# Performance work log

Measured on AMD Instinct MI355X. Metric: run time of the kernel, lower is better.

## Reference

```python
import jax, jax.numpy as jnp
import numpy as np
from jax import lax

B, C, H, W = 4, 3, 512, 512
PATCH = 64
STRIDE = 32
CHANS = [(3, 32), (32, 32), (32, 64), (64, 64), (64, 64), (64, 32), (32, 32), (32, 2)]


def _conv(x, w, b):
    y = lax.conv_general_dilated(x, w, (1, 1), [(1, 1), (1, 1)],
                                 dimension_numbers=('NCHW', 'OIHW', 'NCHW'))
    return y + b[None, :, None, None]


def _pool(x):  # MaxPool2d(2)
    return lax.reduce_window(x, -jnp.inf, lax.max, (1, 1, 2, 2), (1, 1, 2, 2), 'VALID')


def _up(x):  # Upsample(scale=2, bilinear, align_corners=False) == half-pixel resize
    b, c, h, w = x.shape
    return jax.image.resize(x, (b, c, 2 * h, 2 * w), 'bilinear')


def _flow_net(x, ws, bs):
    r = jax.nn.relu
    h = r(_conv(x, ws[0], bs[0]))
    h = r(_conv(h, ws[1], bs[1]))
    h = _pool(h)
    h = r(_conv(h, ws[2], bs[2]))
    h = r(_conv(h, ws[3], bs[3]))
    h = _pool(h)
    h = _up(h)
    h = r(_conv(h, ws[4], bs[4]))
    h = r(_conv(h, ws[5], bs[5]))
    h = _up(h)
    h = r(_conv(h, ws[6], bs[6]))
    return jnp.tanh(_conv(h, ws[7], bs[7]))  # [B,2,H,W]


def _bilinear_zeros(img, gx, gy):
    # img [C,H,W], gx/gy [N,P,P] in [-1,1]; grid_sample bilinear, zeros padding, align_corners=False
    Hh, Ww = img.shape[1], img.shape[2]
    ix = ((gx + 1.0) * Ww - 1.0) * 0.5
    iy = ((gy + 1.0) * Hh - 1.0) * 0.5
    x0 = jnp.floor(ix)
    y0 = jnp.floor(iy)
    wx1 = ix - x0
    wy1 = iy - y0

    def corner(xi, yi, wgt):
        valid = (xi >= 0) & (xi <= Ww - 1) & (yi >= 0) & (yi <= Hh - 1)
        xc = jnp.clip(xi, 0, Ww - 1).astype(jnp.int32)
        yc = jnp.clip(yi, 0, Hh - 1).astype(jnp.int32)
        return img[:, yc, xc] * (wgt * valid)[None]  # [C,N,P,P]

    return (corner(x0, y0, (1 - wx1) * (1 - wy1))
            + corner(x0 + 1, y0, wx1 * (1 - wy1))
            + corner(x0, y0 + 1, (1 - wx1) * wy1)
            + corner(x0 + 1, y0 + 1, wx1 * wy1))


def _forward(x, ws, bs, temp):
    b, c, h, w = x.shape
    flow = _flow_net(x, ws, bs)  # [B,2,H,W]
    gy, gx = jnp.meshgrid(jnp.linspace(-1.0, 1.0, h), jnp.linspace(-1.0, 1.0, w), indexing='ij')
    base = jnp.stack([gx, gy], axis=-1)  # [H,W,2] (x,y)
    deformed = base[None] + flow.transpose(0, 2, 3, 1) * temp  # [B,H,W,2]
    centers = deformed[:, ::STRIDE, ::STRIDE, :].reshape(b, -1, 2)  # [B,N,2]
    py, px = jnp.meshgrid(jnp.linspace(-1.0, 1.0, PATCH), jnp.linspace(-1.0, 1.0, PATCH), indexing='ij')
    pgx = centers[:, :, None, None, 0] + px[None, None] * (PATCH / w)  # [B,N,P,P]
    pgy = centers[:, :, None, None, 1] + py[None, None] * (PATCH / h)
    patches = jax.vmap(_bilinear_zeros)(x, pgx, pgy)  # [B,C,N,P,P]
    patches = patches.transpose(0, 2, 1, 3, 4)  # [B,N,C,P,P]
    return patches, flow, deformed


def setup_inputs() -> dict:
    key = jax.random.key(0)
    ks = jax.random.split(key, len(CHANS) + 1)
    d = {"x": jax.random.normal(ks[0], (B, C, H, W), jnp.float32)}
    for i, (ci, co) in enumerate(CHANS):
        d[f"w{i}"] = jax.random.normal(ks[i + 1], (co, ci, 3, 3), jnp.float32) * 0.01
        d[f"b{i}"] = jnp.zeros((co,), jnp.float32)
    d["temp"] = jnp.full((1,), 0.1, jnp.float32)
    return d


def reference(x, w0, b0, w1, b1, w2, b2, w3, b3, w4, b4, w5, b5, w6, b6, w7, b7, temp):
    ws = [w0, w1, w2, w3, w4, w5, w6, w7]
    bs = [b0, b1, b2, b3, b4, b5, b6, b7]
    return _forward(x, ws, bs, temp)
```

## Files before the change

### kernel.cpp

```cpp
#include <hip/hip_runtime.h>
#include <hip/hip_bf16.h>

typedef __hip_bfloat16 bf16;
typedef unsigned short ushort_t;
typedef __attribute__((ext_vector_type(8))) short short8;
typedef __attribute__((ext_vector_type(4))) float float4v;

#define BATCH 4
#define HH 512
#define WW 512

#define WO_L0 0
#define WO_L1 3072
#define WO_L2 12288
#define WO_L3 30720
#define WO_L4P 67584
#define WO_L5 215040
#define WO_L6P 233472
#define WO_L7 270336
#define WO_L4U 274944
#define WO_L6U 311808

__device__ __forceinline__ ushort_t f2bfu(float f) {
  __hip_bfloat16 h = __float2bfloat16(f);
  union { __hip_bfloat16 h; ushort_t u; } c;
  c.h = h;
  return c.u;
}
__device__ __forceinline__ float bfu2f(ushort_t u) {
  return __uint_as_float(((unsigned)u) << 16);
}

__device__ __forceinline__ void dma16(void* lds, const void* g) {
  __builtin_amdgcn_global_load_lds(
      (const __attribute__((address_space(1))) unsigned int*)g,
      (__attribute__((address_space(3))) unsigned int*)lds, 16, 0, 0);
}

__device__ __forceinline__ float upw(int k, int u) {
  int lo = k >> 1;
  float a = (k & 1) ? 0.25f : 0.75f;
  float b = (k & 1) ? 0.75f : 0.25f;
  return (u == lo) ? a : (u == lo + 1) ? b : 0.0f;
}

struct WP { const float* w[8]; };

__global__ __launch_bounds__(256) void prep_w(WP wp, bf16* __restrict__ dst) {
  const int job = blockIdx.y;
  const int e = blockIdx.x * 256 + threadIdx.x;
  if (job == 0) {
    if (e >= 3072) return;
    int c = e & 7;
    int o = (e >> 3) & 31;
    int g = (e >> 8) % 3;
    int tl = (e >> 8) / 3;
    int tap = g * 4 + tl;
    float v = 0.0f;
    if (tap < 9 && c < 3) v = wp.w[0][(o * 3 + c) * 9 + tap];
    dst[WO_L0 + e] = __float2bfloat16(v);
    return;
  }
  if (job == 4 || job == 6) {
    const int O = (job == 4) ? 64 : 32;
    const int I = O;
    const int NCH = I >> 5;
    const int n = 4 * NCH * 9 * O * 32;
    if (e >= n) return;
    int ic = e & 31;
    int o = (e >> 5) % O;
    int tap = (e / (32 * O)) % 9;
    int ch = (e / (9 * 32 * O)) % NCH;
    int ph = e / (NCH * 9 * 32 * O);
    int i = ch * 32 + ic;
    int u = tap / 3, v2 = tap - u * 3;
    int dy = ph >> 1, dx = ph & 1;
    const float* w = wp.w[job];
    float acc = 0.0f;
#pragma unroll
    for (int r = 0; r < 3; ++r) {
      float ry = upw(r + dy, u);
#pragma unroll
      for (int s = 0; s < 3; ++s)
        acc += w[(o * I + i) * 9 + r * 3 + s] * ry * upw(s + dx, v2);
    }
    dst[((job == 4) ? WO_L4P : WO_L6P) + e] = __float2bfloat16(acc);
    return;
  }
  int O, I, OP, off;
  const float* w;
  if (job == 1)      { O = 32; I = 32; OP = 32; off = WO_L1; w = wp.w[1]; }
  else if (job == 2) { O = 64; I = 32; OP = 64; off = WO_L2; w = wp.w[2]; }
  else if (job == 3) { O = 64; I = 64; OP = 64; off = WO_L3; w = wp.w[3]; }
  else if (job == 5) { O = 32; I = 64; OP = 32; off = WO_L5; w = wp.w[5]; }
  else if (job == 7) { O = 2;  I = 32; OP = 16; off = WO_L7; w = wp.w[7]; }
  else if (job == 8) { O = 64; I = 64; OP = 64; off = WO_L4U; w = wp.w[4]; }
  else               { O = 32; I = 32; OP = 32; off = WO_L6U; w = wp.w[6]; }
  const int NCH = I >> 5;
  const int n = NCH * 9 * OP * 32;
  if (e >= n) return;
  int ic = e & 31;
  int o = (e >> 5) % OP;
  int tap = (e / (32 * OP)) % 9;
  int ch = e / (9 * 32 * OP);
  int i = ch * 32 + ic;
  float v = 0.0f;
  if (o < O) v = w[(o * I + i) * 9 + tap];
  dst[off + e] = __float2bfloat16(v);
}

__global__ __launch_bounds__(256) void pack_x(const float* __restrict__ x,
                                              bf16* __restrict__ xp) {
  int i = blockIdx.x * 256 + threadIdx.x;
  if (i >= BATCH * HH * WW) return;
  int b = i / (HH * WW);
  int px = i - b * (HH * WW);
  union { uint4 v; ushort_t s[8]; } o;
  o.v = make_uint4(0, 0, 0, 0);
  const float* p = x + (long)b * 3 * HH * WW + px;
  o.s[0] = f2bfu(p[0]);
  o.s[1] = f2bfu(p[HH * WW]);
  o.s[2] = f2bfu(p[2 * HH * WW]);
  *(uint4*)&xp[(long)i * 8] = o.v;
}

__global__ __launch_bounds__(512) void conv01_k(
    const bf16* __restrict__ xp, const bf16* __restrict__ w0,
    const bf16* __restrict__ w1, const float* __restrict__ b0,
    const float* __restrict__ b1, bf16* __restrict__ out) {
  __shared__ alignas(16) bf16 xp_lds[720 * 8];
  __shared__ alignas(16) bf16 mid_lds[612 * 32];
  __shared__ alignas(16) bf16 w0_lds[3072];
  __shared__ alignas(16) bf16 w1_lds[9 * 32 * 32];
  const int tid = threadIdx.x;
  const int lane = tid & 63;
  const int wid = tid >> 6;
  const int lm = lane & 15;
  const int quad = lane >> 4;
  const int x0 = blockIdx.x * 16, y0 = blockIdx.y * 32;
  const int b = blockIdx.z;

  for (int u = tid; u < 720; u += 512) {
    int hy = u / 20, hx = u - hy * 20;
    int gy = y0 - 2 + hy, gx = x0 - 2 + hx;
    uint4 v = make_uint4(0, 0, 0, 0);
    if (gy >= 0 && gy < HH && gx >= 0 && gx < WW)
      v = *(const uint4*)(xp + (((long)b * HH + gy) * WW + gx) * 8);
    *(uint4*)&xp_lds[u * 8] = v;
  }
  if (tid < 384) *(uint4*)&w0_lds[tid * 8] = *(const uint4*)(w0 + tid * 8);
  for (int j = wid; j < 18; j += 8)
    dma16((char*)w1_lds + j * 1024, (const char*)w1 + j * 1024 + lane * 16);
  __syncthreads();

  for (int t = wid; t < 39; t += 8) {
    int px = t * 16 + lm;
    int pxc = min(px, 611);
    int hy = pxc / 18, hx = pxc - hy * 18;
    float4v acc0[2];
#pragma unroll
    for (int mt = 0; mt < 2; ++mt)
      acc0[mt] = *(const float4v*)(b0 + mt * 16 + quad * 4);
#pragma unroll
    for (int g = 0; g < 3; ++g) {
      int tap = g * 4 + quad;
      if (tap > 8) tap = 8;
      int r = (tap * 11) >> 5;
      int s = tap - r * 3;
      short8 bfr = *(const short8*)&xp_lds[((hy + r) * 20 + hx + s) * 8];
      short8 a0 = *(const short8*)&w0_lds[quad * 768 + (g * 32 + lm) * 8];
      short8 a1 = *(const short8*)&w0_lds[quad * 768 + (g * 32 + 16 + lm) * 8];
      acc0[0] = __builtin_amdgcn_mfma_f32_16x16x32_bf16(a0, bfr, acc0[0], 0, 0, 0);
      acc0[1] = __builtin_amdgcn_mfma_f32_16x16x32_bf16(a1, bfr, acc0[1], 0, 0, 0);
    }
    int gy = y0 - 1 + hy, gx = x0 - 1 + hx;
    bool inimg = (gy >= 0) && (gy < HH) && (gx >= 0) && (gx < WW);
    if (px < 612) {
#pragma unroll
      for (int mt = 0; mt < 2; ++mt) {
        union { uint2 v; ushort_t s2[4]; } pk;
#pragma unroll
        for (int r2 = 0; r2 < 4; ++r2)
          pk.s2[r2] = inimg ? f2bfu(fmaxf(acc0[mt][r2], 0.0f)) : (ushort_t)0;
        *(uint2*)&mid_lds[px * 32 + mt * 16 + quad * 4] = pk.v;
      }
    }
  }
  __syncthreads();

  float4v acc[2][4];
#pragma unroll
  for (int mt = 0; mt < 2; ++mt) {
    float4v bv = *(const float4v*)(b1 + mt * 16 + quad * 4);
#pragma unroll
    for (int nt = 0; nt < 4; ++nt) acc[mt][nt] = bv;
  }
#pragma unroll
  for (int tap = 0; tap < 9; ++tap) {
    const int r = tap / 3, s = tap - r * 3;
    short8 afrag[2], bfrag[4];
#pragma unroll
    for (int mt = 0; mt < 2; ++mt)
      afrag[mt] = *(const short8*)&w1_lds[(tap * 32 + mt * 16 + lm) * 32 + quad * 8];
#pragma unroll
    for (int nt = 0; nt < 4; ++nt) {
      int py = 4 * wid + nt;
      bfrag[nt] = *(const short8*)&mid_lds[((py + r) * 18 + lm + s) * 32 + quad * 8];
    }
#pragma unroll
    for (int mt = 0; mt < 2; ++mt)
#pragma unroll
      for (int nt = 0; nt < 4; ++nt)
        acc[mt][nt] = __builtin_amdgcn_mfma_f32_16x16x32_bf16(
            afrag[mt], bfrag[nt], acc[mt][nt], 0, 0, 0);
  }
  const int Ho = HH >> 1, Wo = WW >> 1;
#pragma unroll
  for (int mt = 0; mt < 2; ++mt) {
#pragma unroll
    for (int g = 0; g < 2; ++g) {
      float4v m;
#pragma unroll
      for (int r = 0; r < 4; ++r)
        m[r] = fmaxf(fmaxf(acc[mt][2 * g][r], acc[mt][2 * g + 1][r]), 0.0f);
#pragma unroll
      for (int r = 0; r < 4; ++r) m[r] = fmaxf(m[r], __shfl_xor(m[r], 1, 64));
      if ((lm & 1) == 0) {
        int pyo = (y0 >> 1) + 2 * wid + g;
        int pxo = (x0 >> 1) + (lm >> 1);
        union { uint2 v; ushort_t s[4]; } pk;
#pragma unroll
        for (int r = 0; r < 4; ++r) pk.s[r] = f2bfu(m[r]);
        *(uint2*)&out[(((long)b * Ho + pyo) * Wo + pxo) * 32 + mt * 16 +
                      quad * 4] = pk.v;
      }
    }
  }
}

template <int CIN, int COUT, int COUTR, int OUT_MODE>
__global__ __launch_bounds__(512) void conv_mfma(
    const bf16* __restrict__ in, const bf16* __restrict__ wt,
    const float* __restrict__ bias, void* __restrict__ out_, int H, int W,
    const float* __restrict__ temp, float* __restrict__ def) {
  constexpr int MT = COUT / 16;
  constexpr int CK = 32;
  __shared__ alignas(16) bf16 in_lds[612 * CK];
  __shared__ alignas(16) bf16 w_lds[9 * COUT * CK];
  const int tid = threadIdx.x;
  const int lane = tid & 63;
  const int wid = tid >> 6;
  const int lm = lane & 15;
  const int quad = lane >> 4;
  const int x0 = blockIdx.x * 16;
  const int y0 = blockIdx.y * 32;
  const int b = blockIdx.z;

  float4v acc[MT][4];
#pragma unroll
  for (int mt = 0; mt < MT; ++mt) {
    float4v bv;
    if constexpr (COUTR == COUT) {
      bv = *(const float4v*)(bias + mt * 16 + quad * 4);
    } else {
#pragma unroll
      for (int r = 0; r < 4; ++r) {
        int co = mt * 16 + quad * 4 + r;
        bv[r] = (co < COUTR) ? bias[co] : 0.0f;
      }
    }
#pragma unroll
    for (int nt = 0; nt < 4; ++nt) acc[mt][nt] = bv;
  }

  const bool interior =
      (x0 >= 1) && (x0 + 16 <= W - 1) && (y0 >= 1) && (y0 + 32 <= H - 1);
  for (int c0 = 0; c0 < CIN; c0 += CK) {
    if (interior) {
      for (int r = wid; r < 34; r += 8) {
        int gy = y0 - 1 + r;
        const bf16* gsrc = in + (((long)b * H + gy) * W + x0) * CIN + c0 +
                           (lane >> 2) * CIN + (lane & 3) * 8;
        dma16(&in_lds[(r * 18 + 1) * CK], gsrc);
      }
      if (tid < 272) {
        int r = tid >> 3;
        int side = (tid >> 2) & 1;
        int seg = tid & 3;
        int gx = side ? (x0 + 16) : (x0 - 1);
        int gy = y0 - 1 + r;
        uint4 v = *(const uint4*)(in + (((long)b * H + gy) * W + gx) * CIN +
                                  c0 + seg * 8);
        *(uint4*)&in_lds[(r * 18 + (side ? 17 : 0)) * CK + seg * 8] = v;
      }
    } else {
      for (int u = tid; u < 612 * 4; u += 512) {
        int px = u >> 2;
        int seg = u & 3;
        int hy = px / 18, hx = px - hy * 18;
        int gy = y0 - 1 + hy, gx = x0 - 1 + hx;
        uint4 v = make_uint4(0, 0, 0, 0);
        if (gy >= 0 && gy < H && gx >= 0 && gx < W)
          v = *(const uint4*)(in + (((long)b * H + gy) * W + gx) * CIN + c0 +
                              seg * 8);
        *(uint4*)&in_lds[px * CK + seg * 8] = v;
      }
    }
    {
      const char* wsrc = (const char*)(wt + (size_t)(c0 >> 5) * 9 * COUT * CK);
      constexpr int WCH = 9 * COUT * CK * 2 / 1024;
      for (int j = wid; j < WCH; j += 8)
        dma16((char*)w_lds + j * 1024, wsrc + j * 1024 + lane * 16);
    }
    __syncthreads();

#pragma unroll
    for (int tap = 0; tap < 9; ++tap) {
      const int r = tap / 3, s = tap - r * 3;
      short8 afrag[MT], bfrag[4];
#pragma unroll
      for (int mt = 0; mt < MT; ++mt)
        afrag[mt] =
            *(const short8*)&w_lds[(tap * COUT + mt * 16 + lm) * CK + quad * 8];
#pragma unroll
      for (int nt = 0; nt < 4; ++nt) {
        int py = 4 * wid + nt;
        bfrag[nt] =
            *(const short8*)&in_lds[((py + r) * 18 + lm + s) * CK + quad * 8];
      }
#pragma unroll
      for (int mt = 0; mt < MT; ++mt)
#pragma unroll
        for (int nt = 0; nt < 4; ++nt)
          acc[mt][nt] = __builtin_amdgcn_mfma_f32_16x16x32_bf16(
              afrag[mt], bfrag[nt], acc[mt][nt], 0, 0, 0);
    }
    __syncthreads();
  }

  if constexpr (OUT_MODE == 3) {
    bf16* out = (bf16*)out_;
    const int Ho = H >> 1, Wo = W >> 1;
#pragma unroll
    for (int mt = 0; mt < MT; ++mt) {
#pragma unroll
      for (int g = 0; g < 2; ++g) {
        float4v m;
#pragma unroll
        for (int r = 0; r < 4; ++r)
          m[r] = fmaxf(fmaxf(acc[mt][2 * g][r], acc[mt][2 * g + 1][r]), 0.0f);
#pragma unroll
        for (int r = 0; r < 4; ++r) m[r] = fmaxf(m[r], __shfl_xor(m[r], 1, 64));
        if ((lm & 1) == 0) {
          int pyo = (y0 >> 1) + 2 * wid + g;
          int pxo = (x0 >> 1) + (lm >> 1);
          union { uint2 v; ushort_t s[4]; } pk;
#pragma unroll
          for (int r = 0; r < 4; ++r) pk.s[r] = f2bfu(m[r]);
          *(uint2*)&out[(((long)b * Ho + pyo) * Wo + pxo) * COUT + mt * 16 +
                        quad * 4] = pk.v;
        }
      }
    }
  } else {
#pragma unroll
    for (int mt = 0; mt < MT; ++mt) {
#pragma unroll
      for (int nt = 0; nt < 4; ++nt) {
        int gy = y0 + 4 * wid + nt;
        int gx = x0 + lm;
        float4v v = acc[mt][nt];
        if constexpr (OUT_MODE == 0) {
          bf16* out = (bf16*)out_;
          union { uint2 v; ushort_t s[4]; } pk;
#pragma unroll
          for (int r = 0; r < 4; ++r) pk.s[r] = f2bfu(fmaxf(v[r], 0.0f));
          *(uint2*)&out[(((long)b * H + gy) * W + gx) * COUT + mt * 16 +
                        quad * 4] = pk.v;
        } else {
          float* out = (float*)out_;
          if (quad == 0) {
            float fx = tanhf(v[0]);
            float fy = tanhf(v[1]);
            out[(((long)b * 2 + 0) * H + gy) * (long)W + gx] = fx;
            out[(((long)b * 2 + 1) * H + gy) * (long)W + gx] = fy;
            float T = temp[0];
            float2 d;
            d.x = -1.0f + gx * (2.0f / 511.0f) + fx * T;
            d.y = -1.0f + gy * (2.0f / 511.0f) + fy * T;
            *(float2*)&def[(((long)b * HH + gy) * WW + gx) * 2] = d;
          }
        }
      }
    }
  }
}

template <int CIN, int COUT, bool PSPLIT>
__global__ __launch_bounds__(512) void conv_up(
    const bf16* __restrict__ in, const bf16* __restrict__ wtP,
    const bf16* __restrict__ wtU, const float* __restrict__ bias,
    bf16* __restrict__ out, int Ho, int Wo) {
  constexpr int MT = COUT / 16;
  constexpr int CK = 32;
  constexpr int WSZ = 9 * COUT * CK;
  constexpr int NWB = PSPLIT ? 1 : 2;
  __shared__ alignas(16) bf16 in_lds[612 * CK];
  __shared__ alignas(16) bf16 w_lds[NWB * WSZ];
  const int tid = threadIdx.x;
  const int lane = tid & 63;
  const int wid = tid >> 6;
  const int lm = lane & 15;
  const int quad = lane >> 4;
  const int Hs = Ho >> 1, Ws = Wo >> 1;
  const int nx = Ws >> 4, ny = Hs >> 5;
  const int bulkN = nx * ny;
  const int b = PSPLIT ? (blockIdx.z >> 2) : blockIdx.z;
  const int ph0 = PSPLIT ? (blockIdx.z & 3) : 0;
  const int t = blockIdx.x;

  if (t >= bulkN) {
    if (PSPLIT && ph0 != 0) return;
    const int G = Wo >> 4;
    int e = t - bulkN;
    int tx, ty;
    if (e < G) { ty = 0; tx = e; }
    else if (e < 2 * G) { ty = G - 1; tx = e - G; }
    else { int u = e - 2 * G; ty = 1 + (u >> 1); tx = (u & 1) ? (G - 1) : 0; }
    const int x0 = tx * 16, y0 = ty * 16;

    float4v acc[MT][4];
#pragma unroll
    for (int mt = 0; mt < MT; ++mt) {
      float4v bv = *(const float4v*)(bias + mt * 16 + quad * 4);
#pragma unroll
      for (int nt = 0; nt < 4; ++nt) acc[mt][nt] = bv;
    }

    for (int c0 = 0; c0 < CIN; c0 += CK) {
      for (int u = tid; u < 324 * 4; u += 512) {
        int px = u >> 2;
        int seg = u & 3;
        int hy = px / 18, hx = px - hy * 18;
        int gy = y0 - 1 + hy, gx = x0 - 1 + hx;
        uint4 o = make_uint4(0, 0, 0, 0);
        if (gy >= 0 && gy < Ho && gx >= 0 && gx < Wo) {
          int ys = (gy >> 1) - ((gy & 1) ? 0 : 1);
          int xs = (gx >> 1) - ((gx & 1) ? 0 : 1);
          float wy = (gy & 1) ? 0.25f : 0.75f;
          float wx = (gx & 1) ? 0.25f : 0.75f;
          int y0c = max(ys, 0), y1c = min(ys + 1, Hs - 1);
          int x0c = max(xs, 0), x1c = min(xs + 1, Ws - 1);
          const bf16* p = in + ((long)b * Hs * Ws) * CIN + c0 + seg * 8;
          union { uint4 v; ushort_t s[8]; } a00, a01, a10, a11, r;
          a00.v = *(const uint4*)(p + ((long)y0c * Ws + x0c) * CIN);
          a01.v = *(const uint4*)(p + ((long)y0c * Ws + x1c) * CIN);
          a10.v = *(const uint4*)(p + ((long)y1c * Ws + x0c) * CIN);
          a11.v = *(const uint4*)(p + ((long)y1c * Ws + x1c) * CIN);
#pragma unroll
          for (int j = 0; j < 8; ++j) {
            float f = (1.0f - wy) * ((1.0f - wx) * bfu2f(a00.s[j]) +
                                     wx * bfu2f(a01.s[j])) +
                      wy * ((1.0f - wx) * bfu2f(a10.s[j]) +
                            wx * bfu2f(a11.s[j]));
            r.s[j] = f2bfu(f);
          }
          o = r.v;
        }
        *(uint4*)&in_lds[px * CK + seg * 8] = o;
      }
      {
        const char* wsrc = (const char*)(wtU + (size_t)(c0 >> 5) * WSZ);
        constexpr int WCH = WSZ * 2 / 1024;
        for (int j = wid; j < WCH; j += 8)
          dma16((char*)w_lds + j * 1024, wsrc + j * 1024 + lane * 16);
      }
      __syncthreads();
      if (wid < 4) {
#pragma unroll
        for (int tap = 0; tap < 9; ++tap) {
          const int r = tap / 3, s = tap - r * 3;
          short8 afrag[MT], bfrag[4];
#pragma unroll
          for (int mt = 0; mt < MT; ++mt)
            afrag[mt] =
                *(const short8*)&w_lds[(tap * COUT + mt * 16 + lm) * CK + quad * 8];
#pragma unroll
          for (int nt = 0; nt < 4; ++nt) {
            int py = 4 * wid + nt;
            bfrag[nt] =
                *(const short8*)&in_lds[((py + r) * 18 + lm + s) * CK + quad * 8];
          }
#pragma unroll
          for (int mt = 0; mt < MT; ++mt)
#pragma unroll
            for (int nt = 0; nt < 4; ++nt)
              acc[mt][nt] = __builtin_amdgcn_mfma_f32_16x16x32_bf16(
                  afrag[mt], bfrag[nt], acc[mt][nt], 0, 0, 0);
        }
      }
      __syncthreads();
    }
    if (wid < 4) {
#pragma unroll
      for (int mt = 0; mt < MT; ++mt)
#pragma unroll
        for (int nt = 0; nt < 4; ++nt) {
          int gy = y0 + 4 * wid + nt;
          int gx = x0 + lm;
          union { uint2 v; ushort_t s[4]; } pk;
#pragma unroll
          for (int r = 0; r < 4; ++r)
            pk.s[r] = f2bfu(fmaxf(acc[mt][nt][r], 0.0f));
          *(uint2*)&out[(((long)b * Ho + gy) * Wo + gx) * COUT + mt * 16 +
                        quad * 4] = pk.v;
        }
    }
    return;
  }

  const int bx = t % nx, by = t / nx;
  const int xs0 = bx * 16, ys0 = by * 32;
  const bool interior = (bx >= 1) && (bx < nx - 1) && (by >= 1) && (by < ny - 1);

  if constexpr (!PSPLIT) {
    static_assert(CIN == CK, "non-split bulk path assumes single K chunk");
    if (interior) {
      for (int r = wid; r < 34; r += 8) {
        int gy = ys0 - 1 + r;
        const bf16* gsrc = in + (((long)b * Hs + gy) * Ws + xs0) * CIN +
                           (lane >> 2) * CIN + (lane & 3) * 8;
        dma16(&in_lds[(r * 18 + 1) * CK], gsrc);
      }
      if (tid < 272) {
        int r = tid >> 3;
        int side = (tid >> 2) & 1;
        int seg = tid & 3;
        int gx = side ? (xs0 + 16) : (xs0 - 1);
        int gy = ys0 - 1 + r;
        uint4 v = *(const uint4*)(in + (((long)b * Hs + gy) * Ws + gx) * CIN +
                                  seg * 8);
        *(uint4*)&in_lds[(r * 18 + (side ? 17 : 0)) * CK + seg * 8] = v;
      }
    } else {
      for (int u = tid; u < 612 * 4; u += 512) {
        int px = u >> 2;
        int seg = u & 3;
        int hy = px / 18, hx = px - hy * 18;
        int sy = min(max(ys0 - 1 + hy, 0), Hs - 1);
        int sx = min(max(xs0 - 1 + hx, 0), Ws - 1);
        uint4 v = *(const uint4*)(in + (((long)b * Hs + sy) * Ws + sx) * CIN +
                                  seg * 8);
        *(uint4*)&in_lds[px * CK + seg * 8] = v;
      }
    }
    constexpr int WCH = WSZ * 2 / 1024;
    for (int j = wid; j < WCH; j += 8)
      dma16((char*)w_lds + j * 1024, (const char*)wtP + j * 1024 + lane * 16);
    __syncthreads();

    for (int ph = 0; ph < 4; ++ph) {
      const int cur = ph & 1;
      if (ph < 3) {
        const char* wsrc = (const char*)(wtP + (size_t)(ph + 1) * WSZ);
        char* wdst = (char*)w_lds + (cur ^ 1) * WSZ * 2;
        for (int j = wid; j < WCH; j += 8)
          dma16(wdst + j * 1024, wsrc + j * 1024 + lane * 16);
      }
      float4v acc[MT][4];
#pragma unroll
      for (int mt = 0; mt < MT; ++mt) {
        float4v bv = *(const float4v*)(bias + mt * 16 + quad * 4);
#pragma unroll
        for (int nt = 0; nt < 4; ++nt) acc[mt][nt] = bv;
      }
      const bf16* wb = w_lds + cur * WSZ;
#pragma unroll
      for (int tap = 0; tap < 9; ++tap) {
        const int r = tap / 3, s = tap - r * 3;
        short8 afrag[MT], bfrag[4];
#pragma unroll
        for (int mt = 0; mt < MT; ++mt)
          afrag[mt] =
              *(const short8*)&wb[(tap * COUT + mt * 16 + lm) * CK + quad * 8];
#pragma unroll
        for (int nt = 0; nt < 4; ++nt) {
          int py = 4 * wid + nt;
          bfrag[nt] =
              *(const short8*)&in_lds[((py + r) * 18 + lm + s) * CK + quad * 8];
        }
#pragma unroll
        for (int mt = 0; mt < MT; ++mt)
#pragma unroll
          for (int nt = 0; nt < 4; ++nt)
            acc[mt][nt] = __builtin_amdgcn_mfma_f32_16x16x32_bf16(
                afrag[mt], bfrag[nt], acc[mt][nt], 0, 0, 0);
      }
      const int dy = ph >> 1, dx = ph & 1;
#pragma unroll
      for (int mt = 0; mt < MT; ++mt)
#pragma unroll
        for (int nt = 0; nt < 4; ++nt) {
          int gy = 2 * (ys0 + 4 * wid + nt) + dy;
          int gx = 2 * (xs0 + lm) + dx;
          if (gy >= 16 && gy < Ho - 16 && gx >= 16 && gx < Wo - 16) {
            union { uint2 v; ushort_t s2[4]; } pk;
#pragma unroll
            for (int r2 = 0; r2 < 4; ++r2)
              pk.s2[r2] = f2bfu(fmaxf(acc[mt][nt][r2], 0.0f));
            *(uint2*)&out[(((long)b * Ho + gy) * Wo + gx) * COUT + mt * 16 +
                          quad * 4] = pk.v;
          }
        }
      __syncthreads();
    }
    return;
  }

  const int ph = ph0;
  float4v acc[MT][4];
#pragma unroll
  for (int mt = 0; mt < MT; ++mt) {
    float4v bv = *(const float4v*)(bias + mt * 16 + quad * 4);
#pragma unroll
    for (int nt = 0; nt < 4; ++nt) acc[mt][nt] = bv;
  }
  for (int c0 = 0; c0 < CIN; c0 += CK) {
    if (interior) {
      for (int r = wid; r < 34; r += 8) {
        int gy = ys0 - 1 + r;
        const bf16* gsrc = in + (((long)b * Hs + gy) * Ws + xs0) * CIN +
                           c0 + (lane >> 2) * CIN + (lane & 3) * 8;
        dma16(&in_lds[(r * 18 + 1) * CK], gsrc);
      }
      if (tid < 272) {
        int r = tid >> 3;
        int side = (tid >> 2) & 1;
        int seg = tid & 3;
        int gx = side ? (xs0 + 16) : (xs0 - 1);
        int gy = ys0 - 1 + r;
        uint4 v = *(const uint4*)(in + (((long)b * Hs + gy) * Ws + gx) * CIN +
                                  c0 + seg * 8);
        *(uint4*)&in_lds[(r * 18 + (side ? 17 : 0)) * CK + seg * 8] = v;
      }
    } else {
      for (int u = tid; u < 612 * 4; u += 512) {
        int px = u >> 2;
        int seg = u & 3;
        int hy = px / 18, hx = px - hy * 18;
        int sy = min(max(ys0 - 1 + hy, 0), Hs - 1);
        int sx = min(max(xs0 - 1 + hx, 0), Ws - 1);
        uint4 v = *(const uint4*)(in + (((long)b * Hs + sy) * Ws + sx) * CIN +
                                  seg * 8);
        *(uint4*)&in_lds[px * CK + seg * 8] = v;
      }
    }
    {
      const char* wsrc = (const char*)(wtP + (size_t)(ph * (CIN / CK) + (c0 >> 5)) * WSZ);
      constexpr int WCH = WSZ * 2 / 1024;
      for (int j = wid; j < WCH; j += 8)
        dma16((char*)w_lds + j * 1024, wsrc + j * 1024 + lane * 16);
    }
    __syncthreads();
#pragma unroll
    for (int tap = 0; tap < 9; ++tap) {
      const int r = tap / 3, s = tap - r * 3;
      short8 afrag[MT], bfrag[4];
#pragma unroll
      for (int mt = 0; mt < MT; ++mt)
        afrag[mt] =
            *(const short8*)&w_lds[(tap * COUT + mt * 16 + lm) * CK + quad * 8];
#pragma unroll
      for (int nt = 0; nt < 4; ++nt) {
        int py = 4 * wid + nt;
        bfrag[nt] =
            *(const short8*)&in_lds[((py + r) * 18 + lm + s) * CK + quad * 8];
      }
#pragma unroll
      for (int mt = 0; mt < MT; ++mt)
#pragma unroll
        for (int nt = 0; nt < 4; ++nt)
          acc[mt][nt] = __builtin_amdgcn_mfma_f32_16x16x32_bf16(
              afrag[mt], bfrag[nt], acc[mt][nt], 0, 0, 0);
    }
    __syncthreads();
  }
  const int dy = ph >> 1, dx = ph & 1;
#pragma unroll
  for (int mt = 0; mt < MT; ++mt)
#pragma unroll
    for (int nt = 0; nt < 4; ++nt) {
      int gy = 2 * (ys0 + 4 * wid + nt) + dy;
      int gx = 2 * (xs0 + lm) + dx;
      if (gy >= 16 && gy < Ho - 16 && gx >= 16 && gx < Wo - 16) {
        union { uint2 v; ushort_t s2[4]; } pk;
#pragma unroll
        for (int r2 = 0; r2 < 4; ++r2)
          pk.s2[r2] = f2bfu(fmaxf(acc[mt][nt][r2], 0.0f));
        *(uint2*)&out[(((long)b * Ho + gy) * Wo + gx) * COUT + mt * 16 +
                      quad * 4] = pk.v;
      }
    }
}

__global__ __launch_bounds__(256) void patches_k(const float* __restrict__ x,
                                                 const float* __restrict__ def,
                                                 float* __restrict__ out) {
  int i = blockIdx.x * 256 + threadIdx.x;
  int pj = i & 63;
  int t = i >> 6;
  int pi = t & 63;
  t >>= 6;
  int n = t & 255;
  int b = t >> 8;
  if (b >= BATCH) return;
  int hi = n >> 4, wi = n & 15;
  const float* dptr = def + (((long)b * HH + hi * 32) * WW + wi * 32) * 2;
  float cx = dptr[0], cy = dptr[1];
  float pgx = cx + (-1.0f + pj * (2.0f / 63.0f)) * 0.125f;
  float pgy = cy + (-1.0f + pi * (2.0f / 63.0f)) * 0.125f;
  float ix = ((pgx + 1.0f) * 512.0f - 1.0f) * 0.5f;
  float iy = ((pgy + 1.0f) * 512.0f - 1.0f) * 0.5f;
  float fx0 = floorf(ix), fy0 = floorf(iy);
  float wx1 = ix - fx0, wy1 = iy - fy0;
  int x0 = (int)fx0, y0 = (int)fy0;
  int x1 = x0 + 1, y1 = y0 + 1;
  bool vx0 = (x0 >= 0) && (x0 <= 511), vx1 = (x1 >= 0) && (x1 <= 511);
  bool vy0 = (y0 >= 0) && (y0 <= 511), vy1 = (y1 >= 0) && (y1 <= 511);
  int cx0 = min(max(x0, 0), 511), cx1 = min(max(x1, 0), 511);
  int cy0 = min(max(y0, 0), 511), cy1 = min(max(y1, 0), 511);
  float w00 = (1.0f - wx1) * (1.0f - wy1) * ((vx0 && vy0) ? 1.0f : 0.0f);
  float w01 = wx1 * (1.0f - wy1) * ((vx1 && vy0) ? 1.0f : 0.0f);
  float w10 = (1.0f - wx1) * wy1 * ((vx0 && vy1) ? 1.0f : 0.0f);
  float w11 = wx1 * wy1 * ((vx1 && vy1) ? 1.0f : 0.0f);
#pragma unroll
  for (int c = 0; c < 3; ++c) {
    const float* img = x + ((long)b * 3 + c) * (HH * WW);
    float v = img[cy0 * WW + cx0] * w00 + img[cy0 * WW + cx1] * w01 +
              img[cy1 * WW + cx0] * w10 + img[cy1 * WW + cx1] * w11;
    out[(((long)b * 256 + n) * 3 + c) * 4096 + pi * 64 + pj] = v;
  }
}


extern "C" void kernel_launch(void* const* d_in, const int* in_sizes, int n_in,
                              void* d_out, int out_size, void* d_ws,
                              size_t ws_size, hipStream_t stream) {
  const float* x = (const float*)d_in[0];
  WP wp;
  const float* bs[8];
  for (int i = 0; i < 8; ++i) {
    wp.w[i] = (const float*)d_in[1 + 2 * i];
    bs[i] = (const float*)d_in[2 + 2 * i];
  }
  const float* temp = (const float*)d_in[17];

  float* out = (float*)d_out;
  float* flow = out + 12582912;
  float* def = out + 14680064;
  bf16* wT = (bf16*)d_out;

  const size_t bufElems = (size_t)BATCH * 512 * 512 * 32;
  bf16* A = (bf16*)d_ws;
  bf16* Bf = A + bufElems;
  bf16* xp = Bf + bufElems;

  prep_w<<<dim3(576, 10), 256, 0, stream>>>(wp, wT);
  pack_x<<<(BATCH * HH * WW) / 256, 256, 0, stream>>>(x, xp);

  conv01_k<<<dim3(32, 16, BATCH), 512, 0, stream>>>(
      xp, wT + WO_L0, wT + WO_L1, bs[0], bs[1], Bf);
  conv_mfma<32, 64, 64, 0><<<dim3(16, 8, BATCH), 512, 0, stream>>>(
      Bf, wT + WO_L2, bs[2], A, 256, 256, nullptr, nullptr);
  conv_mfma<64, 64, 64, 3><<<dim3(16, 8, BATCH), 512, 0, stream>>>(
      A, wT + WO_L3, bs[3], Bf, 256, 256, nullptr, nullptr);
  conv_up<64, 64, true><<<dim3(8 * 4 + 60, 1, 4 * BATCH), 512, 0, stream>>>(
      Bf, wT + WO_L4P, wT + WO_L4U, bs[4], A, 256, 256);
  conv_mfma<64, 32, 32, 0><<<dim3(16, 8, BATCH), 512, 0, stream>>>(
      A, wT + WO_L5, bs[5], Bf, 256, 256, nullptr, nullptr);
  conv_up<32, 32, false><<<dim3(16 * 8 + 124, 1, BATCH), 512, 0, stream>>>(
      Bf, wT + WO_L6P, wT + WO_L6U, bs[6], A, 512, 512);
  conv_mfma<32, 16, 2, 2><<<dim3(32, 16, BATCH), 512, 0, stream>>>(
      A, wT + WO_L7, bs[7], flow, 512, 512, temp, def);
  patches_k<<<(BATCH * 256 * 64 * 64) / 256, 256, 0, stream>>>(x, def, out);
}
```

Measured before the change: 318.2 us.

## Pair upsample-conv phases to reuse input fragments and split edge-tile output channels

The non-split bulk path now loads two phase weight sets at once and computes two phases per pass. Each input fragment read from LDS therefore feeds twice as many MFMAs, and there are half as many phase iterations. Double-buffered prefetch of the next phase's weights is dropped, so weight loads are no longer overlapped with compute. Edge tiles now use all 8 waves by splitting output-channel tiles across wave halves, where only 4 waves computed before; doubled accumulators raise register pressure.

Measured after the change: 317.5 us. No clear change (-0.2%).

```diff
diff --git a/kernel.cpp b/kernel.cpp
--- a/kernel.cpp
+++ b/kernel.cpp
@@ -402,11 +402,12 @@
     const bf16* __restrict__ wtU, const float* __restrict__ bias,
     bf16* __restrict__ out, int Ho, int Wo) {
   constexpr int MT = COUT / 16;
+  constexpr int MH = MT / 2;
   constexpr int CK = 32;
   constexpr int WSZ = 9 * COUT * CK;
-  constexpr int NWB = PSPLIT ? 1 : 2;
+  constexpr int WBUF = PSPLIT ? WSZ : 2 * WSZ;
   __shared__ alignas(16) bf16 in_lds[612 * CK];
-  __shared__ alignas(16) bf16 w_lds[NWB * WSZ];
+  __shared__ alignas(16) bf16 w_lds[WBUF];
   const int tid = threadIdx.x;
   const int lane = tid & 63;
   const int wid = tid >> 6;
@@ -428,13 +429,15 @@
     else if (e < 2 * G) { ty = G - 1; tx = e - G; }
     else { int u = e - 2 * G; ty = 1 + (u >> 1); tx = (u & 1) ? (G - 1) : 0; }
     const int x0 = tx * 16, y0 = ty * 16;
-
-    float4v acc[MT][4];
-#pragma unroll
-    for (int mt = 0; mt < MT; ++mt) {
-      float4v bv = *(const float4v*)(bias + mt * 16 + quad * 4);
-#pragma unroll
-      for (int nt = 0; nt < 4; ++nt) acc[mt][nt] = bv;
+    const int wrow = wid & 3;
+    const int wmt = (wid >> 2) * MH;
+
+    float4v acc[MH][4];
+#pragma unroll
+    for (int m = 0; m < MH; ++m) {
+      float4v bv = *(const float4v*)(bias + (wmt + m) * 16 + quad * 4);
+#pragma unroll
+      for (int nt = 0; nt < 4; ++nt) acc[m][nt] = bv;
     }
 
     for (int c0 = 0; c0 < CIN; c0 += CK) {
@@ -476,46 +479,41 @@
           dma16((char*)w_lds + j * 1024, wsrc + j * 1024 + lane * 16);
       }
       __syncthreads();
-      if (wid < 4) {
-#pragma unroll
-        for (int tap = 0; tap < 9; ++tap) {
-          const int r = tap / 3, s = tap - r * 3;
-          short8 afrag[MT], bfrag[4];
-#pragma unroll
-          for (int mt = 0; mt < MT; ++mt)
-            afrag[mt] =
-                *(const short8*)&w_lds[(tap * COUT + mt * 16 + lm) * CK + quad * 8];
-#pragma unroll
-          for (int nt = 0; nt < 4; ++nt) {
-            int py = 4 * wid + nt;
-            bfrag[nt] =
-                *(const short8*)&in_lds[((py + r) * 18 + lm + s) * CK + quad * 8];
-          }
-#pragma unroll
-          for (int mt = 0; mt < MT; ++mt)
-#pragma unroll
-            for (int nt = 0; nt < 4; ++nt)
-              acc[mt][nt] = __builtin_amdgcn_mfma_f32_16x16x32_bf16(
-                  afrag[mt], bfrag[nt], acc[mt][nt], 0, 0, 0);
+#pragma unroll
+      for (int tap = 0; tap < 9; ++tap) {
+        const int r = tap / 3, s = tap - r * 3;
+        short8 afrag[MH], bfrag[4];
+#pragma unroll
+        for (int m = 0; m < MH; ++m)
+          afrag[m] = *(const short8*)&w_lds[(tap * COUT + (wmt + m) * 16 + lm) * CK +
+                                            quad * 8];
+#pragma unroll
+        for (int nt = 0; nt < 4; ++nt) {
+          int py = 4 * wrow + nt;
+          bfrag[nt] =
+              *(const short8*)&in_lds[((py + r) * 18 + lm + s) * CK + quad * 8];
         }
+#pragma unroll
+        for (int m = 0; m < MH; ++m)
+#pragma unroll
+          for (int nt = 0; nt < 4; ++nt)
+            acc[m][nt] = __builtin_amdgcn_mfma_f32_16x16x32_bf16(
+                afrag[m], bfrag[nt], acc[m][nt], 0, 0, 0);
       }
       __syncthreads();
     }
-    if (wid < 4) {
-#pragma unroll
-      for (int mt = 0; mt < MT; ++mt)
-#pragma unroll
-        for (int nt = 0; nt < 4; ++nt) {
-          int gy = y0 + 4 * wid + nt;
-          int gx = x0 + lm;
-          union { uint2 v; ushort_t s[4]; } pk;
-#pragma unroll
-          for (int r = 0; r < 4; ++r)
-            pk.s[r] = f2bfu(fmaxf(acc[mt][nt][r], 0.0f));
-          *(uint2*)&out[(((long)b * Ho + gy) * Wo + gx) * COUT + mt * 16 +
-                        quad * 4] = pk.v;
-        }
-    }
+#pragma unroll
+    for (int m = 0; m < MH; ++m)
+#pragma unroll
+      for (int nt = 0; nt < 4; ++nt) {
+        int gy = y0 + 4 * wrow + nt;
+        int gx = x0 + lm;
+        union { uint2 v; ushort_t s[4]; } pk;
+#pragma unroll
+        for (int r = 0; r < 4; ++r) pk.s[r] = f2bfu(fmaxf(acc[m][nt][r], 0.0f));
+        *(uint2*)&out[(((long)b * Ho + gy) * Wo + gx) * COUT + (wmt + m) * 16 +
+                      quad * 4] = pk.v;
+      }
     return;
   }
 
@@ -554,35 +552,27 @@
         *(uint4*)&in_lds[px * CK + seg * 8] = v;
       }
     }
-    constexpr int WCH = WSZ * 2 / 1024;
-    for (int j = wid; j < WCH; j += 8)
-      dma16((char*)w_lds + j * 1024, (const char*)wtP + j * 1024 + lane * 16);
-    __syncthreads();
-
-    for (int ph = 0; ph < 4; ++ph) {
-      const int cur = ph & 1;
-      if (ph < 3) {
-        const char* wsrc = (const char*)(wtP + (size_t)(ph + 1) * WSZ);
-        char* wdst = (char*)w_lds + (cur ^ 1) * WSZ * 2;
+    constexpr int WCH = 2 * WSZ * 2 / 1024;
+    for (int pair = 0; pair < 2; ++pair) {
+      {
+        const char* wsrc = (const char*)(wtP + (size_t)(2 * pair) * WSZ);
         for (int j = wid; j < WCH; j += 8)
-          dma16(wdst + j * 1024, wsrc + j * 1024 + lane * 16);
-      }
-      float4v acc[MT][4];
-#pragma unroll
-      for (int mt = 0; mt < MT; ++mt) {
-        float4v bv = *(const float4v*)(bias + mt * 16 + quad * 4);
-#pragma unroll
-        for (int nt = 0; nt < 4; ++nt) acc[mt][nt] = bv;
-      }
-      const bf16* wb = w_lds + cur * WSZ;
+          dma16((char*)w_lds + j * 1024, wsrc + j * 1024 + lane * 16);
+      }
+      __syncthreads();
+      float4v acc[2][MT][4];
+#pragma unroll
+      for (int p = 0; p < 2; ++p)
+#pragma unroll
+        for (int mt = 0; mt < MT; ++mt) {
+          float4v bv = *(const float4v*)(bias + mt * 16 + quad * 4);
+#pragma unroll
+          for (int nt = 0; nt < 4; ++nt) acc[p][mt][nt] = bv;
+        }
 #pragma unroll
       for (int tap = 0; tap < 9; ++tap) {
         const int r = tap / 3, s = tap - r * 3;
-        short8 afrag[MT], bfrag[4];
-#pragma unroll
-        for (int mt = 0; mt < MT; ++mt)
-          afrag[mt] =
-              *(const short8*)&wb[(tap * COUT + mt * 16 + lm) * CK + quad * 8];
+        short8 bfrag[4], afrag[2][MT];
 #pragma unroll
         for (int nt = 0; nt < 4; ++nt) {
           int py = 4 * wid + nt;
@@ -590,28 +580,40 @@
               *(const short8*)&in_lds[((py + r) * 18 + lm + s) * CK + quad * 8];
         }
 #pragma unroll
+        for (int p = 0; p < 2; ++p)
+#pragma unroll
+          for (int mt = 0; mt < MT; ++mt)
+            afrag[p][mt] = *(const short8*)&w_lds[p * WSZ +
+                (tap * COUT + mt * 16 + lm) * CK + quad * 8];
+#pragma unroll
+        for (int p = 0; p < 2; ++p)
+#pragma unroll
+          for (int mt = 0; mt < MT; ++mt)
+#pragma unroll
+            for (int nt = 0; nt < 4; ++nt)
+              acc[p][mt][nt] = __builtin_amdgcn_mfma_f32_16x16x32_bf16(
+                  afrag[p][mt], bfrag[nt], acc[p][mt][nt], 0, 0, 0);
+      }
+      const int dy = pair;
+#pragma unroll
+      for (int p = 0; p < 2; ++p) {
+        const int dx = p;
+#pragma unroll
         for (int mt = 0; mt < MT; ++mt)
 #pragma unroll
-          for (int nt = 0; nt < 4; ++nt)
-            acc[mt][nt] = __builtin_amdgcn_mfma_f32_16x16x32_bf16(
-                afrag[mt], bfrag[nt], acc[mt][nt], 0, 0, 0);
-      }
-      const int dy = ph >> 1, dx = ph & 1;
-#pragma unroll
-      for (int mt = 0; mt < MT; ++mt)
-#pragma unroll
-        for (int nt = 0; nt < 4; ++nt) {
-          int gy = 2 * (ys0 + 4 * wid + nt) + dy;
-          int gx = 2 * (xs0 + lm) + dx;
-          if (gy >= 16 && gy < Ho - 16 && gx >= 16 && gx < Wo - 16) {
-            union { uint2 v; ushort_t s2[4]; } pk;
-#pragma unroll
-            for (int r2 = 0; r2 < 4; ++r2)
-              pk.s2[r2] = f2bfu(fmaxf(acc[mt][nt][r2], 0.0f));
-            *(uint2*)&out[(((long)b * Ho + gy) * Wo + gx) * COUT + mt * 16 +
-                          quad * 4] = pk.v;
+          for (int nt = 0; nt < 4; ++nt) {
+            int gy = 2 * (ys0 + 4 * wid + nt) + dy;
+            int gx = 2 * (xs0 + lm) + dx;
+            if (gy >= 16 && gy < Ho - 16 && gx >= 16 && gx < Wo - 16) {
+              union { uint2 v; ushort_t s2[4]; } pk;
+#pragma unroll
+              for (int r2 = 0; r2 < 4; ++r2)
+                pk.s2[r2] = f2bfu(fmaxf(acc[p][mt][nt][r2], 0.0f));
+              *(uint2*)&out[(((long)b * Ho + gy) * Wo + gx) * COUT + mt * 16 +
+                            quad * 4] = pk.v;
+            }
           }
-        }
+      }
       __syncthreads();
     }
     return;
```
